# Optimization experiments

Hardware: AMD Instinct MI355X
Metric: run time of the kernel (lower is better)

## Reference

```python
import jax, jax.numpy as jnp
import numpy as np

NUM_HEADS = 8
EPS = 1e-12  # matches torch F.normalize eps


def setup_inputs() -> dict:
    key = jax.random.key(0)
    ks = jax.random.split(key, 4)
    B, C, H, W = 32, 384, 32, 32
    x = jax.random.normal(ks[0], (B, C, H, W), dtype=jnp.float32)
    w_qkv = jax.random.normal(ks[1], (3 * C, C), dtype=jnp.float32) * (1.0 / np.sqrt(C))
    b_qkv = jnp.zeros((3 * C,), dtype=jnp.float32)
    temperature = jnp.ones((NUM_HEADS, 1, 1), dtype=jnp.float32)
    w_proj = jax.random.normal(ks[2], (C, C), dtype=jnp.float32) * (1.0 / np.sqrt(C))
    b_proj = jnp.zeros((C,), dtype=jnp.float32)
    return {"x": x, "w_qkv": w_qkv, "b_qkv": b_qkv, "temperature": temperature,
            "w_proj": w_proj, "b_proj": b_proj}


def _l2norm_tokens(t):
    # L2-normalize over the token axis N (last dim), torch F.normalize semantics
    n = jnp.sqrt(jnp.sum(t * t, axis=-1, keepdims=True))
    return t / jnp.maximum(n, EPS)


def reference(x, w_qkv, b_qkv, temperature, w_proj, b_proj):
    B, C, H, W = x.shape
    N = H * W
    nh = NUM_HEADS
    dh = C // nh
    xf = x.reshape(B, C, N)
    # 1x1 conv == channel GEMM: [B,3C,N]
    qkv = jnp.einsum('oc,bcn->bon', w_qkv, xf) + b_qkv[:, None]
    qkv = qkv.reshape(B, 3, nh, dh, N)
    q, k, v = qkv[:, 0], qkv[:, 1], qkv[:, 2]  # each [B,nh,dh,N]
    q = _l2norm_tokens(q)
    k = _l2norm_tokens(k)
    # cross-covariance: contract over N -> small [B,nh,dh,dh]
    attn = jnp.einsum('bhdn,bhen->bhde', q, k) * temperature
    attn = jax.nn.softmax(attn, axis=-1)
    out = jnp.einsum('bhde,bhen->bhdn', attn, v).reshape(B, C, N)
    out = jnp.einsum('oc,bcn->bon', w_proj, out) + b_proj[:, None]
    return x + out.reshape(B, C, H, W)
```

## Files before the change

### kernel.cpp

```cpp
#include <hip/hip_runtime.h>
#include <hip/hip_bf16.h>
#include <stdint.h>

#define BATCH  32
#define CDIM   384
#define NTOK   1024
#define NHEADS 8
#define DH     48

using f32x4  = __attribute__((ext_vector_type(4))) float;
using bf16x8 = __attribute__((ext_vector_type(8))) short;
using u16x4  = __attribute__((ext_vector_type(4))) uint16_t;

__device__ __forceinline__ uint16_t f2bf(float f) {
  uint32_t x = __float_as_uint(f);
  uint32_t r = (x + 0x7fffu + ((x >> 16) & 1u)) >> 16;
  return (uint16_t)r;
}
__device__ __forceinline__ float bf2f(uint16_t u) {
  return __uint_as_float(((uint32_t)u) << 16);
}

#define GLL16(gsrc, ldst)                                                    \
  __builtin_amdgcn_global_load_lds(                                          \
      (const __attribute__((address_space(1))) void*)(gsrc),                 \
      (__attribute__((address_space(3))) void*)(ldst), 16, 0, 0)

__global__ __launch_bounds__(256) void k_transpose_x(const float* __restrict__ x,
                                                     uint16_t* __restrict__ xT) {
  __shared__ float t[32][33];
  int tid = threadIdx.x;
  int n0 = blockIdx.x * 32;
  int c0 = blockIdx.y * 32;
  int b  = blockIdx.z;
  const float* xb = x + (size_t)b * CDIM * NTOK;
#pragma unroll
  for (int p = 0; p < 4; ++p) {
    int idx = tid + p * 256;
    int i = idx >> 5, j = idx & 31;
    t[i][j] = xb[(size_t)(c0 + i) * NTOK + n0 + j];
  }
  __syncthreads();
  uint16_t* xTb = xT + (size_t)b * NTOK * CDIM;
#pragma unroll
  for (int p = 0; p < 4; ++p) {
    int idx = tid + p * 256;
    int jj = idx >> 5, ii = idx & 31;
    xTb[(size_t)(n0 + jj) * CDIM + c0 + ii] = f2bf(t[ii][jj]);
  }
}

__global__ __launch_bounds__(256) void k_convert_w(const float* __restrict__ wqkv,
                                                   const float* __restrict__ wproj,
                                                   uint16_t* __restrict__ wq,
                                                   uint16_t* __restrict__ wp) {
  int n1 = 3 * CDIM * CDIM;
  int n2 = CDIM * CDIM;
  int stride = gridDim.x * 256;
  for (int i = blockIdx.x * 256 + threadIdx.x; i < n1 + n2; i += stride) {
    if (i < n1) wq[i] = f2bf(wqkv[i]);
    else        wp[i - n1] = f2bf(wproj[i - n1]);
  }
}

__device__ __forceinline__ void gemm_tile_128(const uint16_t* __restrict__ A,
                                              const uint16_t* __restrict__ B,
                                              uint16_t* ldsA, uint16_t* ldsB,
                                              f32x4 acc[4][4], int tid) {
  const int K = 384;
  int w = tid >> 6, lane = tid & 63;
  int wr = w >> 1, wc = w & 1;
  int lr = lane & 15, g = lane >> 4;
  for (int kt = 0; kt < K; kt += 64) {
    __syncthreads();
#pragma unroll
    for (int iss = 0; iss < 4; ++iss) {
      int ch = tid + 256 * iss;
      int r  = ch >> 3;
      int cs = (((ch & 7) ^ (r & 7)) << 3);
      GLL16(A + (size_t)r * K + kt + cs, ldsA + (size_t)ch * 8);
      GLL16(B + (size_t)r * K + kt + cs, ldsB + (size_t)ch * 8);
    }
    __syncthreads();
#pragma unroll
    for (int ks = 0; ks < 2; ++ks) {
      bf16x8 af[4], bfr[4];
#pragma unroll
      for (int mt = 0; mt < 4; ++mt) {
        int row = wr * 64 + mt * 16 + lr;
        int sl  = (((ks * 4 + g) ^ (row & 7)) << 3);
        af[mt] = *(const bf16x8*)(ldsA + (size_t)row * 64 + sl);
      }
#pragma unroll
      for (int nt = 0; nt < 4; ++nt) {
        int row = wc * 64 + nt * 16 + lr;
        int sl  = (((ks * 4 + g) ^ (row & 7)) << 3);
        bfr[nt] = *(const bf16x8*)(ldsB + (size_t)row * 64 + sl);
      }
#pragma unroll
      for (int mt = 0; mt < 4; ++mt)
#pragma unroll
        for (int nt = 0; nt < 4; ++nt)
          acc[mt][nt] = __builtin_amdgcn_mfma_f32_16x16x32_bf16(af[mt], bfr[nt], acc[mt][nt], 0, 0, 0);
    }
  }
}

__global__ __launch_bounds__(256) void k_qkv(const uint16_t* __restrict__ Wq,
                                             const uint16_t* __restrict__ xT,
                                             const float* __restrict__ bqkv,
                                             uint16_t* __restrict__ qk,
                                             uint16_t* __restrict__ vT) {
  __shared__ uint16_t ldsA[128 * 64];
  __shared__ uint16_t ldsB[128 * 64];
  int tid = threadIdx.x;
  int jt = blockIdx.x, bm = blockIdx.y;
  int o0 = bm * 128, j0 = jt * 128;
  f32x4 acc[4][4];
#pragma unroll
  for (int i = 0; i < 4; ++i)
#pragma unroll
    for (int j = 0; j < 4; ++j) acc[i][j] = (f32x4){0.f, 0.f, 0.f, 0.f};

  gemm_tile_128(Wq + (size_t)o0 * 384, xT + (size_t)j0 * 384, ldsA, ldsB, acc, tid);

  int w = tid >> 6, lane = tid & 63;
  int wr = w >> 1, wc = w & 1, lr = lane & 15, g = lane >> 4;
#pragma unroll
  for (int mt = 0; mt < 4; ++mt) {
    int ob = o0 + wr * 64 + mt * 16 + g * 4;
    float b0 = bqkv[ob + 0], b1 = bqkv[ob + 1], b2 = bqkv[ob + 2], b3 = bqkv[ob + 3];
#pragma unroll
    for (int nt = 0; nt < 4; ++nt) {
      int j = j0 + wc * 64 + nt * 16 + lr;
      int b = j >> 10, n = j & 1023;
      f32x4 v = acc[mt][nt];
      float v0 = v[0] + b0, v1 = v[1] + b1, v2 = v[2] + b2, v3 = v[3] + b3;
      if (ob < 768) {
        uint16_t* dst = qk + ((size_t)(b * 768 + ob) * 1024 + n);
        dst[0] = f2bf(v0); dst[1024] = f2bf(v1); dst[2048] = f2bf(v2); dst[3072] = f2bf(v3);
      } else {
        int oc = ob - 768;
        int h = oc / 48, d = oc % 48;
        u16x4 p;
        p[0] = f2bf(v0); p[1] = f2bf(v1); p[2] = f2bf(v2); p[3] = f2bf(v3);
        *(u16x4*)(vT + ((size_t)((b * 8 + h) * 1024 + n) * 48 + d)) = p;
      }
    }
  }
}

__global__ __launch_bounds__(256) void k_attn(const uint16_t* __restrict__ qk,
                                              const uint16_t* __restrict__ vT,
                                              const float* __restrict__ temperature,
                                              uint16_t* __restrict__ aT) {
  __shared__ float Sp[4][48][49];
  __shared__ float Sf[48][49];
  __shared__ uint16_t P[48][72];
  __shared__ float nrm[96];
  int tid = threadIdx.x, w = tid >> 6, lane = tid & 63;
  int bh = blockIdx.x, b = bh >> 3, h = bh & 7;
  const uint16_t* qbase = qk + (size_t)(b * 768 + h * 48) * 1024;
  const uint16_t* kbase = qbase + (size_t)384 * 1024;

  for (int r = w; r < 96; r += 4) {
    const uint16_t* row = (r < 48) ? (qbase + (size_t)r * 1024)
                                   : (kbase + (size_t)(r - 48) * 1024);
    float s = 0.f;
#pragma unroll
    for (int jj = 0; jj < 4; ++jj) {
      u16x4 u = *(const u16x4*)(row + (size_t)(jj * 64 + lane) * 4);
#pragma unroll
      for (int e = 0; e < 4; ++e) { float f = bf2f(u[e]); s += f * f; }
    }
#pragma unroll
    for (int off = 32; off > 0; off >>= 1) s += __shfl_down(s, off);
    if (lane == 0) nrm[r] = fmaxf(sqrtf(s), 1e-12f);
  }

  int lr = lane & 15, g = lane >> 4;
  int nbase = w * 256;
  f32x4 sacc[3][3];
#pragma unroll
  for (int i = 0; i < 3; ++i)
#pragma unroll
    for (int j = 0; j < 3; ++j) sacc[i][j] = (f32x4){0.f, 0.f, 0.f, 0.f};
#pragma unroll
  for (int ks = 0; ks < 8; ++ks) {
    bf16x8 aq[3], bk[3];
#pragma unroll
    for (int mt = 0; mt < 3; ++mt)
      aq[mt] = *(const bf16x8*)(qbase + (size_t)(mt * 16 + lr) * 1024 + nbase + ks * 32 + g * 8);
#pragma unroll
    for (int et = 0; et < 3; ++et)
      bk[et] = *(const bf16x8*)(kbase + (size_t)(et * 16 + lr) * 1024 + nbase + ks * 32 + g * 8);
#pragma unroll
    for (int mt = 0; mt < 3; ++mt)
#pragma unroll
      for (int et = 0; et < 3; ++et)
        sacc[mt][et] = __builtin_amdgcn_mfma_f32_16x16x32_bf16(aq[mt], bk[et], sacc[mt][et], 0, 0, 0);
  }
#pragma unroll
  for (int mt = 0; mt < 3; ++mt)
#pragma unroll
    for (int et = 0; et < 3; ++et)
#pragma unroll
      for (int r = 0; r < 4; ++r)
        Sp[w][mt * 16 + g * 4 + r][et * 16 + lr] = sacc[mt][et][r];
  __syncthreads();

  float temp = temperature[h];
  for (int idx = tid; idx < 48 * 48; idx += 256) {
    int d = idx / 48, e = idx - d * 48;
    float s = Sp[0][d][e] + Sp[1][d][e] + Sp[2][d][e] + Sp[3][d][e];
    Sf[d][e] = s * temp / (nrm[d] * nrm[48 + e]);
  }
  __syncthreads();

  if (tid < 48) {
    int d = tid;
    float m = -1e30f;
    for (int e = 0; e < 48; ++e) m = fmaxf(m, Sf[d][e]);
    float sum = 0.f;
    for (int e = 0; e < 48; ++e) { float v = __expf(Sf[d][e] - m); sum += v; Sf[d][e] = v; }
    float inv = 1.f / sum;
    for (int e = 0; e < 48; ++e) P[d][e] = f2bf(Sf[d][e] * inv);
    for (int e = 48; e < 64; ++e) P[d][e] = 0;
  }
  __syncthreads();

  bf16x8 af[3][2];
#pragma unroll
  for (int mt = 0; mt < 3; ++mt)
#pragma unroll
    for (int ks = 0; ks < 2; ++ks)
      af[mt][ks] = *(const bf16x8*)(&P[mt * 16 + lr][ks * 32 + g * 8]);
  const uint16_t* vb = vT + (size_t)(b * 8 + h) * 1024 * 48;
  bf16x8 zf;
#pragma unroll
  for (int i = 0; i < 8; ++i) zf[i] = 0;
#pragma unroll 4
  for (int nt = 0; nt < 16; ++nt) {
    int n = w * 256 + nt * 16 + lr;
    bf16x8 bv[2];
    bv[0] = *(const bf16x8*)(vb + (size_t)n * 48 + g * 8);
    int eb1 = 32 + g * 8;
    bv[1] = (eb1 < 48) ? *(const bf16x8*)(vb + (size_t)n * 48 + eb1) : zf;
    f32x4 o[3];
#pragma unroll
    for (int mt = 0; mt < 3; ++mt) o[mt] = (f32x4){0.f, 0.f, 0.f, 0.f};
#pragma unroll
    for (int ks = 0; ks < 2; ++ks)
#pragma unroll
      for (int mt = 0; mt < 3; ++mt)
        o[mt] = __builtin_amdgcn_mfma_f32_16x16x32_bf16(af[mt][ks], bv[ks], o[mt], 0, 0, 0);
#pragma unroll
    for (int mt = 0; mt < 3; ++mt) {
      int c = h * 48 + mt * 16 + g * 4;
      u16x4 p;
#pragma unroll
      for (int r = 0; r < 4; ++r) p[r] = f2bf(o[mt][r]);
      *(u16x4*)(aT + ((size_t)(b * 1024 + n) * 384 + c)) = p;
    }
  }
}

__global__ __launch_bounds__(256) void k_proj(const uint16_t* __restrict__ Wp,
                                              const uint16_t* __restrict__ aT,
                                              const float* __restrict__ bproj,
                                              const float* __restrict__ x,
                                              float* __restrict__ out) {
  __shared__ uint16_t ldsA[128 * 64];
  __shared__ uint16_t ldsB[128 * 64];
  int tid = threadIdx.x;
  int jt = blockIdx.x, bm = blockIdx.y;
  int o0 = bm * 128, j0 = jt * 128;
  f32x4 acc[4][4];
#pragma unroll
  for (int i = 0; i < 4; ++i)
#pragma unroll
    for (int j = 0; j < 4; ++j) acc[i][j] = (f32x4){0.f, 0.f, 0.f, 0.f};

  gemm_tile_128(Wp + (size_t)o0 * 384, aT + (size_t)j0 * 384, ldsA, ldsB, acc, tid);

  int w = tid >> 6, lane = tid & 63;
  int wr = w >> 1, wc = w & 1, lr = lane & 15, g = lane >> 4;
#pragma unroll
  for (int mt = 0; mt < 4; ++mt) {
    int ob = o0 + wr * 64 + mt * 16 + g * 4;
    float b0 = bproj[ob + 0], b1 = bproj[ob + 1], b2 = bproj[ob + 2], b3 = bproj[ob + 3];
#pragma unroll
    for (int nt = 0; nt < 4; ++nt) {
      int j = j0 + wc * 64 + nt * 16 + lr;
      int b = j >> 10, n = j & 1023;
      f32x4 v = acc[mt][nt];
      size_t i0 = (size_t)(b * 384 + ob) * 1024 + n;
      out[i0]        = v[0] + b0 + x[i0];
      out[i0 + 1024] = v[1] + b1 + x[i0 + 1024];
      out[i0 + 2048] = v[2] + b2 + x[i0 + 2048];
      out[i0 + 3072] = v[3] + b3 + x[i0 + 3072];
    }
  }
}

extern "C" void kernel_launch(void* const* d_in, const int* in_sizes, int n_in,
                              void* d_out, int out_size, void* d_ws, size_t ws_size,
                              hipStream_t stream) {
  const float* x     = (const float*)d_in[0];
  const float* wqkv  = (const float*)d_in[1];
  const float* bqkv  = (const float*)d_in[2];
  const float* temp  = (const float*)d_in[3];
  const float* wproj = (const float*)d_in[4];
  const float* bproj = (const float*)d_in[5];
  float* out = (float*)d_out;

  char* ws = (char*)d_ws;
  size_t off = 0;
  auto alloc = [&](size_t bytes) -> char* {
    char* p = ws + off;
    off += (bytes + 255) & ~(size_t)255;
    return p;
  };
  uint16_t* xT    = (uint16_t*)alloc((size_t)BATCH * NTOK * CDIM * 2);
  uint16_t* wq_bf = (uint16_t*)alloc((size_t)3 * CDIM * CDIM * 2);
  uint16_t* wp_bf = (uint16_t*)alloc((size_t)CDIM * CDIM * 2);
  uint16_t* qkbuf = (uint16_t*)alloc((size_t)BATCH * 768 * NTOK * 2);
  uint16_t* vTbuf = (uint16_t*)alloc((size_t)BATCH * NHEADS * NTOK * DH * 2);
  uint16_t* aT    = xT;

  k_transpose_x<<<dim3(NTOK / 32, CDIM / 32, BATCH), dim3(256), 0, stream>>>(x, xT);
  k_convert_w<<<dim3(576), dim3(256), 0, stream>>>(wqkv, wproj, wq_bf, wp_bf);
  k_qkv<<<dim3(256, 9), dim3(256), 0, stream>>>(wq_bf, xT, bqkv, qkbuf, vTbuf);
  k_attn<<<dim3(256), dim3(256), 0, stream>>>(qkbuf, vTbuf, temp, aT);
  k_proj<<<dim3(256, 3), dim3(256), 0, stream>>>(wp_bf, aT, bproj, x, out);
}
```

Before: 129.2 us.

## Double-buffer GEMM LDS tiles and vectorize the x transpose kernel

The shared GEMM tile routine now uses two LDS buffers so the global-to-LDS loads for the next K slice are issued while MFMAs run on the current one, with one barrier per stage instead of two. The input transpose now works on 64x64 tiles using float4 loads and 16-byte bf16 stores in place of scalar accesses. The double buffering doubles LDS per block to 64 KB, which may lower occupancy, and the full vmcnt(0) wait after each compute limits how much load latency is hidden.

```diff
diff --git a/kernel.cpp b/kernel.cpp
--- a/kernel.cpp
+++ b/kernel.cpp
@@ -11,6 +11,7 @@
 using f32x4  = __attribute__((ext_vector_type(4))) float;
 using bf16x8 = __attribute__((ext_vector_type(8))) short;
 using u16x4  = __attribute__((ext_vector_type(4))) uint16_t;
+using u16x8  = __attribute__((ext_vector_type(8))) uint16_t;
 
 __device__ __forceinline__ uint16_t f2bf(float f) {
   uint32_t x = __float_as_uint(f);
@@ -28,25 +29,29 @@
 
 __global__ __launch_bounds__(256) void k_transpose_x(const float* __restrict__ x,
                                                      uint16_t* __restrict__ xT) {
-  __shared__ float t[32][33];
+  __shared__ float t[64][65];
   int tid = threadIdx.x;
-  int n0 = blockIdx.x * 32;
-  int c0 = blockIdx.y * 32;
+  int n0 = blockIdx.x * 64;
+  int c0 = blockIdx.y * 64;
   int b  = blockIdx.z;
   const float* xb = x + (size_t)b * CDIM * NTOK;
 #pragma unroll
   for (int p = 0; p < 4; ++p) {
-    int idx = tid + p * 256;
-    int i = idx >> 5, j = idx & 31;
-    t[i][j] = xb[(size_t)(c0 + i) * NTOK + n0 + j];
+    int r  = (tid >> 4) + p * 16;
+    int cc = (tid & 15) * 4;
+    float4 v = *(const float4*)(xb + (size_t)(c0 + r) * NTOK + n0 + cc);
+    t[r][cc + 0] = v.x; t[r][cc + 1] = v.y; t[r][cc + 2] = v.z; t[r][cc + 3] = v.w;
   }
   __syncthreads();
   uint16_t* xTb = xT + (size_t)b * NTOK * CDIM;
 #pragma unroll
-  for (int p = 0; p < 4; ++p) {
-    int idx = tid + p * 256;
-    int jj = idx >> 5, ii = idx & 31;
-    xTb[(size_t)(n0 + jj) * CDIM + c0 + ii] = f2bf(t[ii][jj]);
+  for (int p = 0; p < 2; ++p) {
+    int n  = (tid >> 3) + p * 32;
+    int cb = (tid & 7) * 8;
+    u16x8 o;
+#pragma unroll
+    for (int j = 0; j < 8; ++j) o[j] = f2bf(t[cb + j][n]);
+    *(u16x8*)(xTb + (size_t)(n0 + n) * CDIM + c0 + cb) = o;
   }
 }
 
@@ -63,46 +68,70 @@
   }
 }
 
+__device__ __forceinline__ void stage64(const uint16_t* __restrict__ A,
+                                        const uint16_t* __restrict__ B,
+                                        uint16_t* lA, uint16_t* lB,
+                                        int kt, int tid) {
+#pragma unroll
+  for (int iss = 0; iss < 4; ++iss) {
+    int ch = tid + 256 * iss;
+    int r  = ch >> 3;
+    int cs = (((ch & 7) ^ (r & 7)) << 3);
+    GLL16(A + (size_t)r * 384 + kt + cs, lA + (size_t)ch * 8);
+    GLL16(B + (size_t)r * 384 + kt + cs, lB + (size_t)ch * 8);
+  }
+}
+
+__device__ __forceinline__ void compute64(const uint16_t* lA, const uint16_t* lB,
+                                          f32x4 acc[4][4],
+                                          int wr, int wc, int lr, int g) {
+#pragma unroll
+  for (int ks = 0; ks < 2; ++ks) {
+    bf16x8 af[4], bfr[4];
+#pragma unroll
+    for (int mt = 0; mt < 4; ++mt) {
+      int row = wr * 64 + mt * 16 + lr;
+      int sl  = (((ks * 4 + g) ^ (row & 7)) << 3);
+      af[mt] = *(const bf16x8*)(lA + (size_t)row * 64 + sl);
+    }
+#pragma unroll
+    for (int nt = 0; nt < 4; ++nt) {
+      int row = wc * 64 + nt * 16 + lr;
+      int sl  = (((ks * 4 + g) ^ (row & 7)) << 3);
+      bfr[nt] = *(const bf16x8*)(lB + (size_t)row * 64 + sl);
+    }
+#pragma unroll
+    for (int mt = 0; mt < 4; ++mt)
+#pragma unroll
+      for (int nt = 0; nt < 4; ++nt)
+        acc[mt][nt] = __builtin_amdgcn_mfma_f32_16x16x32_bf16(af[mt], bfr[nt], acc[mt][nt], 0, 0, 0);
+  }
+}
+
 __device__ __forceinline__ void gemm_tile_128(const uint16_t* __restrict__ A,
                                               const uint16_t* __restrict__ B,
-                                              uint16_t* ldsA, uint16_t* ldsB,
+                                              uint16_t* lds,
                                               f32x4 acc[4][4], int tid) {
-  const int K = 384;
   int w = tid >> 6, lane = tid & 63;
-  int wr = w >> 1, wc = w & 1;
-  int lr = lane & 15, g = lane >> 4;
-  for (int kt = 0; kt < K; kt += 64) {
-    __syncthreads();
-#pragma unroll
-    for (int iss = 0; iss < 4; ++iss) {
-      int ch = tid + 256 * iss;
-      int r  = ch >> 3;
-      int cs = (((ch & 7) ^ (r & 7)) << 3);
-      GLL16(A + (size_t)r * K + kt + cs, ldsA + (size_t)ch * 8);
-      GLL16(B + (size_t)r * K + kt + cs, ldsB + (size_t)ch * 8);
-    }
-    __syncthreads();
-#pragma unroll
-    for (int ks = 0; ks < 2; ++ks) {
-      bf16x8 af[4], bfr[4];
-#pragma unroll
-      for (int mt = 0; mt < 4; ++mt) {
-        int row = wr * 64 + mt * 16 + lr;
-        int sl  = (((ks * 4 + g) ^ (row & 7)) << 3);
-        af[mt] = *(const bf16x8*)(ldsA + (size_t)row * 64 + sl);
-      }
-#pragma unroll
-      for (int nt = 0; nt < 4; ++nt) {
-        int row = wc * 64 + nt * 16 + lr;
-        int sl  = (((ks * 4 + g) ^ (row & 7)) << 3);
-        bfr[nt] = *(const bf16x8*)(ldsB + (size_t)row * 64 + sl);
-      }
-#pragma unroll
-      for (int mt = 0; mt < 4; ++mt)
-#pragma unroll
-        for (int nt = 0; nt < 4; ++nt)
-          acc[mt][nt] = __builtin_amdgcn_mfma_f32_16x16x32_bf16(af[mt], bfr[nt], acc[mt][nt], 0, 0, 0);
-    }
+  int wr = w >> 1, wc = w & 1, lr = lane & 15, g = lane >> 4;
+  uint16_t* A0 = lds;
+  uint16_t* B0 = lds + 8192;
+  uint16_t* A1 = lds + 16384;
+  uint16_t* B1 = lds + 24576;
+
+  stage64(A, B, A0, B0, 0, tid);
+  asm volatile("s_waitcnt vmcnt(0)" ::: "memory");
+  __builtin_amdgcn_s_barrier();
+#pragma unroll
+  for (int kt = 0; kt < 384; kt += 128) {
+    if (kt + 64 < 384) stage64(A, B, A1, B1, kt + 64, tid);
+    compute64(A0, B0, acc, wr, wc, lr, g);
+    asm volatile("s_waitcnt vmcnt(0)" ::: "memory");
+    __builtin_amdgcn_s_barrier();
+    if (kt + 128 < 384) stage64(A, B, A0, B0, kt + 128, tid);
+    if (kt + 64 < 384) compute64(A1, B1, acc, wr, wc, lr, g);
+    asm volatile("s_waitcnt vmcnt(0)" ::: "memory");
+    __builtin_amdgcn_s_barrier();
   }
 }
 
@@ -111,8 +140,7 @@
                                              const float* __restrict__ bqkv,
                                              uint16_t* __restrict__ qk,
                                              uint16_t* __restrict__ vT) {
-  __shared__ uint16_t ldsA[128 * 64];
-  __shared__ uint16_t ldsB[128 * 64];
+  __shared__ uint16_t lds[4 * 8192];
   int tid = threadIdx.x;
   int jt = blockIdx.x, bm = blockIdx.y;
   int o0 = bm * 128, j0 = jt * 128;
@@ -122,7 +150,7 @@
 #pragma unroll
     for (int j = 0; j < 4; ++j) acc[i][j] = (f32x4){0.f, 0.f, 0.f, 0.f};
 
-  gemm_tile_128(Wq + (size_t)o0 * 384, xT + (size_t)j0 * 384, ldsA, ldsB, acc, tid);
+  gemm_tile_128(Wq + (size_t)o0 * 384, xT + (size_t)j0 * 384, lds, acc, tid);
 
   int w = tid >> 6, lane = tid & 63;
   int wr = w >> 1, wc = w & 1, lr = lane & 15, g = lane >> 4;
@@ -270,8 +298,7 @@
                                               const float* __restrict__ bproj,
                                               const float* __restrict__ x,
                                               float* __restrict__ out) {
-  __shared__ uint16_t ldsA[128 * 64];
-  __shared__ uint16_t ldsB[128 * 64];
+  __shared__ uint16_t lds[4 * 8192];
   int tid = threadIdx.x;
   int jt = blockIdx.x, bm = blockIdx.y;
   int o0 = bm * 128, j0 = jt * 128;
@@ -281,7 +308,7 @@
 #pragma unroll
     for (int j = 0; j < 4; ++j) acc[i][j] = (f32x4){0.f, 0.f, 0.f, 0.f};
 
-  gemm_tile_128(Wp + (size_t)o0 * 384, aT + (size_t)j0 * 384, ldsA, ldsB, acc, tid);
+  gemm_tile_128(Wp + (size_t)o0 * 384, aT + (size_t)j0 * 384, lds, acc, tid);
 
   int w = tid >> 6, lane = tid & 63;
   int wr = w >> 1, wc = w & 1, lr = lane & 15, g = lane >> 4;
@@ -328,7 +355,7 @@
   uint16_t* vTbuf = (uint16_t*)alloc((size_t)BATCH * NHEADS * NTOK * DH * 2);
   uint16_t* aT    = xT;
 
-  k_transpose_x<<<dim3(NTOK / 32, CDIM / 32, BATCH), dim3(256), 0, stream>>>(x, xT);
+  k_transpose_x<<<dim3(NTOK / 64, CDIM / 64, BATCH), dim3(256), 0, stream>>>(x, xT);
   k_convert_w<<<dim3(576), dim3(256), 0, stream>>>(wqkv, wproj, wq_bf, wp_bf);
   k_qkv<<<dim3(256, 9), dim3(256), 0, stream>>>(wq_bf, xT, bqkv, qkbuf, vTbuf);
   k_attn<<<dim3(256), dim3(256), 0, stream>>>(qkbuf, vTbuf, temp, aT);
```

After: 131.8 us. +2.0%, slower.
